# Kernel optimization log

Hardware: AMD Instinct MI355X
Metric: run time of the kernel (lower is better)

## Reference

```python
import jax, jax.numpy as jnp
import numpy as np

E, T, A, H = 64, 128, 32, 4
S, O, QH1, QD, C1 = 256, 128, 128, 64, 128  # state, obs, query hidden, query/key dim, c hidden


def setup_inputs() -> dict:
    key = jax.random.key(0)
    ks = jax.random.split(key, 10)
    w = 0.02
    return {
        "q_values": jax.random.normal(ks[0], (E, T, A), jnp.float32),
        "states": jax.random.normal(ks[1], (E, T, S), jnp.float32),
        "individual_fs": jax.random.normal(ks[2], (E, T, A, O), jnp.float32),
        "Wq1": jax.random.normal(ks[3], (S, QH1), jnp.float32) * w,
        "bq1": jnp.zeros((QH1,), jnp.float32),
        "Wq2": jax.random.normal(ks[4], (QH1, QD), jnp.float32) * w,
        "bq2": jnp.zeros((QD,), jnp.float32),
        "Wk": jax.random.normal(ks[5], (H, O, QD), jnp.float32) * w,
        "bk": jnp.zeros((H, QD), jnp.float32),
        "Wc1": jax.random.normal(ks[6], (S, C1), jnp.float32) * w,
        "bc1": jnp.zeros((C1,), jnp.float32),
        "Wc2": jax.random.normal(ks[7], (C1, 1), jnp.float32) * w,
        "bc2": jnp.zeros((1,), jnp.float32),
    }


def reference(q_values, states, individual_fs, Wq1, bq1, Wq2, bq2, Wk, bk, Wc1, bc1, Wc2, bc2):
    e, t, a = q_values.shape
    s = states.reshape(-1, states.shape[-1])              # (B, S), B = E*T
    f = individual_fs.reshape(e * t, a, -1)               # (B, A, O)
    # query embedding of state: 2-layer MLP with ReLU
    emb_s = jnp.maximum(s @ Wq1 + bq1, 0.0) @ Wq2 + bq2   # (B, QD)
    # all-agents, all-heads key extraction in one batched einsum
    emb_u = jnp.einsum('bao,hok->bahk', f, Wk) + bk       # (B, A, H, QD)
    # query-key dot products per agent/head, then sum over heads
    Lambda_i = jnp.einsum('bk,bahk->bah', emb_s, emb_u).sum(axis=-1)  # (B, A)
    # state-dependent scalar bias
    c_value = jnp.maximum(s @ Wc1 + bc1, 0.0) @ Wc2 + bc2  # (B, 1)
    Q_tot = jnp.sum(Lambda_i * q_values.reshape(-1, a), axis=-1, keepdims=True) + c_value
    return Q_tot.reshape(e, t, 1)
```

## Files before the change

### kernel.cpp

```cpp
#include <hip/hip_runtime.h>


static constexpr int Sd  = 256;
static constexpr int Ad  = 32;
static constexpr int Od  = 128;
static constexpr int QH  = 128;
static constexpr int QDd = 64;
static constexpr int C1d = 128;
static constexpr int NB  = 16;

__global__ void qatten_prep(const float* __restrict__ Wk, const float* __restrict__ bk,
                            float* __restrict__ WkT, float* __restrict__ bkSum)
{
    int idx = blockIdx.x * 256 + threadIdx.x;
    int k = idx >> 7;
    int o = idx & 127;
    float s = 0.f;
#pragma unroll
    for (int h = 0; h < 4; ++h) s += Wk[h * (Od * QDd) + o * QDd + k];
    WkT[k * Od + o] = s;
    if (idx < QDd) {
        float t = 0.f;
#pragma unroll
        for (int h = 0; h < 4; ++h) t += bk[h * QDd + idx];
        bkSum[idx] = t;
    }
}

__global__ __launch_bounds__(256) void qatten_main(
    const float* __restrict__ qv, const float* __restrict__ st, const float* __restrict__ fs,
    const float* __restrict__ Wq1, const float* __restrict__ bq1,
    const float* __restrict__ Wq2, const float* __restrict__ bq2,
    const float* __restrict__ Wc1, const float* __restrict__ bc1,
    const float* __restrict__ Wc2, const float* __restrict__ bc2,
    const float* __restrict__ WkT, const float* __restrict__ bkSum,
    float* __restrict__ out)
{
    __shared__ float s_lds[NB][Sd];
    __shared__ float h1_lds[NB][QH];
    __shared__ float hc_lds[NB][C1d];
    __shared__ float emb_lds[NB][QDd];
    __shared__ float v_lds[NB][Od];
    __shared__ float q_lds[NB][Ad];
    __shared__ float bias_lds[NB];
    __shared__ float part_lds[NB][256];

    const int tid = threadIdx.x;
    const int b0 = blockIdx.x * NB;

    {
        const float4* sp = (const float4*)(st + (size_t)b0 * Sd);
        float4* sl = (float4*)&s_lds[0][0];
#pragma unroll
        for (int i = 0; i < (NB * Sd / 4) / 256; ++i)
            sl[tid + i * 256] = sp[tid + i * 256];
        const float* qp = qv + (size_t)b0 * Ad;
        float* ql = &q_lds[0][0];
#pragma unroll
        for (int i = 0; i < (NB * Ad) / 256; ++i)
            ql[tid + i * 256] = qp[tid + i * 256];
    }
    __syncthreads();

    {
        const int j = tid & 127;
        const bool isC = tid >= 128;
        const float* W  = isC ? Wc1 : Wq1;
        const float* bb = isC ? bc1 : bq1;
        float acc[NB];
#pragma unroll
        for (int b = 0; b < NB; ++b) acc[b] = 0.f;
        for (int i = 0; i < Sd; i += 4) {
            const float w0 = W[(i + 0) * 128 + j];
            const float w1 = W[(i + 1) * 128 + j];
            const float w2 = W[(i + 2) * 128 + j];
            const float w3 = W[(i + 3) * 128 + j];
#pragma unroll
            for (int b = 0; b < NB; ++b) {
                const float4 sv = *(const float4*)&s_lds[b][i];
                float a = acc[b];
                a = fmaf(sv.x, w0, a);
                a = fmaf(sv.y, w1, a);
                a = fmaf(sv.z, w2, a);
                a = fmaf(sv.w, w3, a);
                acc[b] = a;
            }
        }
        const float bias = bb[j];
        float* dst = isC ? &hc_lds[0][0] : &h1_lds[0][0];
#pragma unroll
        for (int b = 0; b < NB; ++b)
            dst[b * 128 + j] = fmaxf(acc[b] + bias, 0.f);
    }
    __syncthreads();

    {
        const int k = tid & 63;
        const int bg = tid >> 6;
        float acc[4] = {0.f, 0.f, 0.f, 0.f};
        for (int j = 0; j < QH; ++j) {
            const float w = Wq2[j * QDd + k];
#pragma unroll
            for (int r = 0; r < 4; ++r)
                acc[r] = fmaf(h1_lds[bg + 4 * r][j], w, acc[r]);
        }
        const float bias = bq2[k];
#pragma unroll
        for (int r = 0; r < 4; ++r)
            emb_lds[bg + 4 * r][k] = acc[r] + bias;
    }
    __syncthreads();

    {
        const int o = tid & 127;
        const int bg = tid >> 7;
        float acc[8] = {0.f,0.f,0.f,0.f,0.f,0.f,0.f,0.f};
        for (int k = 0; k < QDd; ++k) {
            const float w = WkT[k * Od + o];
#pragma unroll
            for (int r = 0; r < 8; ++r)
                acc[r] = fmaf(emb_lds[bg + 2 * r][k], w, acc[r]);
        }
#pragma unroll
        for (int r = 0; r < 8; ++r)
            v_lds[bg + 2 * r][o] = acc[r];
    }
    __syncthreads();

    {
        const int b = tid >> 4;
        const int i = tid & 15;
        float pb = 0.f, pc = 0.f, pq = 0.f;
#pragma unroll
        for (int k = i; k < QDd; k += 16) pb = fmaf(emb_lds[b][k], bkSum[k], pb);
#pragma unroll
        for (int j = i; j < C1d; j += 16) pc = fmaf(hc_lds[b][j], Wc2[j], pc);
        pq = q_lds[b][i] + q_lds[b][i + 16];
#pragma unroll
        for (int d = 8; d >= 1; d >>= 1) {
            pb += __shfl_down(pb, d, 16);
            pc += __shfl_down(pc, d, 16);
            pq += __shfl_down(pq, d, 16);
        }
        if (i == 0) bias_lds[b] = (pc + bc2[0]) + pb * pq;
    }
    __syncthreads();

    {
        const int oq = tid & 31;
        const int ag = tid >> 5;
#pragma unroll 4
        for (int b = 0; b < NB; ++b) {
            const float4* fb = (const float4*)(fs + ((size_t)(b0 + b)) * (Ad * Od));
            const float4 v4 = *(const float4*)&v_lds[b][oq * 4];
            float accb = 0.f;
#pragma unroll
            for (int r = 0; r < 4; ++r) {
                const int a = ag + 8 * r;
                const float4 f4 = fb[a * 32 + oq];
                const float dot = f4.x * v4.x + f4.y * v4.y + f4.z * v4.z + f4.w * v4.w;
                accb = fmaf(q_lds[b][a], dot, accb);
            }
            part_lds[b][tid] = accb;
        }
    }
    __syncthreads();

    {
        const int b = tid >> 4;
        const int i = tid & 15;
        float sum = 0.f;
#pragma unroll
        for (int c = i; c < 256; c += 16) sum += part_lds[b][c];
#pragma unroll
        for (int d = 8; d >= 1; d >>= 1) sum += __shfl_down(sum, d, 16);
        if (i == 0) out[b0 + b] = sum + bias_lds[b];
    }
}

extern "C" void kernel_launch(void* const* d_in, const int* in_sizes, int n_in,
                              void* d_out, int out_size, void* d_ws, size_t ws_size,
                              hipStream_t stream) {
    const float* qv  = (const float*)d_in[0];
    const float* st  = (const float*)d_in[1];
    const float* fs  = (const float*)d_in[2];
    const float* Wq1 = (const float*)d_in[3];
    const float* bq1 = (const float*)d_in[4];
    const float* Wq2 = (const float*)d_in[5];
    const float* bq2 = (const float*)d_in[6];
    const float* Wk  = (const float*)d_in[7];
    const float* bk  = (const float*)d_in[8];
    const float* Wc1 = (const float*)d_in[9];
    const float* bc1 = (const float*)d_in[10];
    const float* Wc2 = (const float*)d_in[11];
    const float* bc2 = (const float*)d_in[12];
    float* out = (float*)d_out;

    float* WkT   = (float*)d_ws;
    float* bkSum = WkT + QDd * Od;

    qatten_prep<<<32, 256, 0, stream>>>(Wk, bk, WkT, bkSum);
    qatten_main<<<512, 256, 0, stream>>>(qv, st, fs, Wq1, bq1, Wq2, bq2,
                                         Wc1, bc1, Wc2, bc2, WkT, bkSum, out);
}
```

Measured before the change: 264.9 us.

## Split fused kernel into MLP kernel and bandwidth-bound feature streaming kernel

The single fused kernel is split into two. The first runs the state MLPs with 32 rows per block and register tiling of two or four columns per thread, then writes the per-row key vectors and scalar bias to workspace. The second streams the large individual_fs tensor with 8 rows per block across 1024 blocks, so more blocks are in flight for the memory-bound part. The cost is an extra launch and a small round trip through global memory for the intermediate vectors.

```diff
diff --git a/kernel.cpp b/kernel.cpp
--- a/kernel.cpp
+++ b/kernel.cpp
@@ -4,10 +4,12 @@
 static constexpr int Sd  = 256;
 static constexpr int Ad  = 32;
 static constexpr int Od  = 128;
-static constexpr int QH  = 128;
 static constexpr int QDd = 64;
-static constexpr int C1d = 128;
-static constexpr int NB  = 16;
+
+static constexpr size_t WS_WKT   = 0;
+static constexpr size_t WS_BKSUM = 8192;
+static constexpr size_t WS_BIAS  = 8256;
+static constexpr size_t WS_V     = 16448;
 
 __global__ void qatten_prep(const float* __restrict__ Wk, const float* __restrict__ bk,
                             float* __restrict__ WkT, float* __restrict__ bkSum)
@@ -27,154 +29,211 @@
     }
 }
 
-__global__ __launch_bounds__(256) void qatten_main(
-    const float* __restrict__ qv, const float* __restrict__ st, const float* __restrict__ fs,
+__global__ __launch_bounds__(256) void qatten_mlp(
+    const float* __restrict__ qv, const float* __restrict__ st,
     const float* __restrict__ Wq1, const float* __restrict__ bq1,
     const float* __restrict__ Wq2, const float* __restrict__ bq2,
     const float* __restrict__ Wc1, const float* __restrict__ bc1,
     const float* __restrict__ Wc2, const float* __restrict__ bc2,
     const float* __restrict__ WkT, const float* __restrict__ bkSum,
+    float* __restrict__ v_ws, float* __restrict__ bias_ws)
+{
+    __shared__ float s_lds[32][Sd];
+    __shared__ float h_lds[32][260];
+    __shared__ float emb_lds[32][QDd];
+
+    const int tid = threadIdx.x;
+    const int b0 = blockIdx.x * 32;
+
+    {
+        const float4* sp = (const float4*)(st + (size_t)b0 * Sd);
+        float4* sl = (float4*)&s_lds[0][0];
+#pragma unroll
+        for (int i = 0; i < 8; ++i) sl[tid + i * 256] = sp[tid + i * 256];
+    }
+    __syncthreads();
+
+    {
+        const int jq = tid & 127;
+        const int rg = tid >> 7;
+        const int c2 = jq * 2;
+        const float* W  = (c2 < 128) ? (Wq1 + c2) : (Wc1 + (c2 - 128));
+        const float* bb = (c2 < 128) ? (bq1 + c2) : (bc1 + (c2 - 128));
+        float acc0[16], acc1[16];
+#pragma unroll
+        for (int r = 0; r < 16; ++r) { acc0[r] = 0.f; acc1[r] = 0.f; }
+        for (int i = 0; i < Sd; i += 4) {
+            const float2 w0 = *(const float2*)(W + (size_t)(i + 0) * 128);
+            const float2 w1 = *(const float2*)(W + (size_t)(i + 1) * 128);
+            const float2 w2 = *(const float2*)(W + (size_t)(i + 2) * 128);
+            const float2 w3 = *(const float2*)(W + (size_t)(i + 3) * 128);
+#pragma unroll
+            for (int r = 0; r < 16; ++r) {
+                const float4 sv = *(const float4*)&s_lds[rg * 16 + r][i];
+                float a0 = acc0[r], a1 = acc1[r];
+                a0 = fmaf(sv.x, w0.x, a0);  a1 = fmaf(sv.x, w0.y, a1);
+                a0 = fmaf(sv.y, w1.x, a0);  a1 = fmaf(sv.y, w1.y, a1);
+                a0 = fmaf(sv.z, w2.x, a0);  a1 = fmaf(sv.z, w2.y, a1);
+                a0 = fmaf(sv.w, w3.x, a0);  a1 = fmaf(sv.w, w3.y, a1);
+                acc0[r] = a0; acc1[r] = a1;
+            }
+        }
+        const float bv0 = bb[0], bv1 = bb[1];
+#pragma unroll
+        for (int r = 0; r < 16; ++r) {
+            float2 hv;
+            hv.x = fmaxf(acc0[r] + bv0, 0.f);
+            hv.y = fmaxf(acc1[r] + bv1, 0.f);
+            *(float2*)&h_lds[rg * 16 + r][c2] = hv;
+        }
+    }
+    __syncthreads();
+
+    {
+        const int jq = tid & 15;
+        const int rg = tid >> 4;
+        const int c4 = jq * 4;
+        float acc[2][4] = {};
+        for (int i = 0; i < 128; i += 4) {
+            const float4 w0 = *(const float4*)(Wq2 + (size_t)(i + 0) * 64 + c4);
+            const float4 w1 = *(const float4*)(Wq2 + (size_t)(i + 1) * 64 + c4);
+            const float4 w2 = *(const float4*)(Wq2 + (size_t)(i + 2) * 64 + c4);
+            const float4 w3 = *(const float4*)(Wq2 + (size_t)(i + 3) * 64 + c4);
+#pragma unroll
+            for (int r = 0; r < 2; ++r) {
+                const float4 hv = *(const float4*)&h_lds[rg * 2 + r][i];
+                acc[r][0] = fmaf(hv.x, w0.x, acc[r][0]);
+                acc[r][1] = fmaf(hv.x, w0.y, acc[r][1]);
+                acc[r][2] = fmaf(hv.x, w0.z, acc[r][2]);
+                acc[r][3] = fmaf(hv.x, w0.w, acc[r][3]);
+                acc[r][0] = fmaf(hv.y, w1.x, acc[r][0]);
+                acc[r][1] = fmaf(hv.y, w1.y, acc[r][1]);
+                acc[r][2] = fmaf(hv.y, w1.z, acc[r][2]);
+                acc[r][3] = fmaf(hv.y, w1.w, acc[r][3]);
+                acc[r][0] = fmaf(hv.z, w2.x, acc[r][0]);
+                acc[r][1] = fmaf(hv.z, w2.y, acc[r][1]);
+                acc[r][2] = fmaf(hv.z, w2.z, acc[r][2]);
+                acc[r][3] = fmaf(hv.z, w2.w, acc[r][3]);
+                acc[r][0] = fmaf(hv.w, w3.x, acc[r][0]);
+                acc[r][1] = fmaf(hv.w, w3.y, acc[r][1]);
+                acc[r][2] = fmaf(hv.w, w3.z, acc[r][2]);
+                acc[r][3] = fmaf(hv.w, w3.w, acc[r][3]);
+            }
+        }
+        const float4 bias = *(const float4*)(bq2 + c4);
+#pragma unroll
+        for (int r = 0; r < 2; ++r) {
+            float4 ev;
+            ev.x = acc[r][0] + bias.x;
+            ev.y = acc[r][1] + bias.y;
+            ev.z = acc[r][2] + bias.z;
+            ev.w = acc[r][3] + bias.w;
+            *(float4*)&emb_lds[rg * 2 + r][c4] = ev;
+        }
+    }
+    __syncthreads();
+
+    {
+        const int jq = tid & 63;
+        const int rg = tid >> 6;
+        const int c2 = jq * 2;
+        float acc0[8], acc1[8];
+#pragma unroll
+        for (int r = 0; r < 8; ++r) { acc0[r] = 0.f; acc1[r] = 0.f; }
+        for (int i = 0; i < QDd; i += 4) {
+            const float2 w0 = *(const float2*)(WkT + (size_t)(i + 0) * 128 + c2);
+            const float2 w1 = *(const float2*)(WkT + (size_t)(i + 1) * 128 + c2);
+            const float2 w2 = *(const float2*)(WkT + (size_t)(i + 2) * 128 + c2);
+            const float2 w3 = *(const float2*)(WkT + (size_t)(i + 3) * 128 + c2);
+#pragma unroll
+            for (int r = 0; r < 8; ++r) {
+                const float4 ev = *(const float4*)&emb_lds[rg * 8 + r][i];
+                float a0 = acc0[r], a1 = acc1[r];
+                a0 = fmaf(ev.x, w0.x, a0);  a1 = fmaf(ev.x, w0.y, a1);
+                a0 = fmaf(ev.y, w1.x, a0);  a1 = fmaf(ev.y, w1.y, a1);
+                a0 = fmaf(ev.z, w2.x, a0);  a1 = fmaf(ev.z, w2.y, a1);
+                a0 = fmaf(ev.w, w3.x, a0);  a1 = fmaf(ev.w, w3.y, a1);
+                acc0[r] = a0; acc1[r] = a1;
+            }
+        }
+#pragma unroll
+        for (int r = 0; r < 8; ++r) {
+            float2 vv; vv.x = acc0[r]; vv.y = acc1[r];
+            *(float2*)(v_ws + (size_t)(b0 + rg * 8 + r) * 128 + c2) = vv;
+        }
+    }
+
+    {
+        const int b = tid >> 3;
+        const int i = tid & 7;
+        float pb = 0.f, pc = 0.f, pq = 0.f;
+#pragma unroll
+        for (int k = i; k < QDd; k += 8)  pb = fmaf(emb_lds[b][k], bkSum[k], pb);
+#pragma unroll
+        for (int j = i; j < 128; j += 8)  pc = fmaf(h_lds[b][128 + j], Wc2[j], pc);
+#pragma unroll
+        for (int a = i; a < Ad; a += 8)   pq += qv[(size_t)(b0 + b) * Ad + a];
+#pragma unroll
+        for (int d = 4; d >= 1; d >>= 1) {
+            pb += __shfl_down(pb, d, 8);
+            pc += __shfl_down(pc, d, 8);
+            pq += __shfl_down(pq, d, 8);
+        }
+        if (i == 0) bias_ws[b0 + b] = (pc + bc2[0]) + pb * pq;
+    }
+}
+
+__global__ __launch_bounds__(256) void qatten_stream(
+    const float* __restrict__ qv, const float* __restrict__ fs,
+    const float* __restrict__ v_ws, const float* __restrict__ bias_ws,
     float* __restrict__ out)
 {
-    __shared__ float s_lds[NB][Sd];
-    __shared__ float h1_lds[NB][QH];
-    __shared__ float hc_lds[NB][C1d];
-    __shared__ float emb_lds[NB][QDd];
-    __shared__ float v_lds[NB][Od];
-    __shared__ float q_lds[NB][Ad];
-    __shared__ float bias_lds[NB];
-    __shared__ float part_lds[NB][256];
+    __shared__ float v_lds[8][Od];
+    __shared__ float q_lds[8][Ad];
+    __shared__ float part_lds[8][256];
 
     const int tid = threadIdx.x;
-    const int b0 = blockIdx.x * NB;
-
-    {
-        const float4* sp = (const float4*)(st + (size_t)b0 * Sd);
-        float4* sl = (float4*)&s_lds[0][0];
-#pragma unroll
-        for (int i = 0; i < (NB * Sd / 4) / 256; ++i)
-            sl[tid + i * 256] = sp[tid + i * 256];
-        const float* qp = qv + (size_t)b0 * Ad;
-        float* ql = &q_lds[0][0];
-#pragma unroll
-        for (int i = 0; i < (NB * Ad) / 256; ++i)
-            ql[tid + i * 256] = qp[tid + i * 256];
-    }
-    __syncthreads();
-
-    {
-        const int j = tid & 127;
-        const bool isC = tid >= 128;
-        const float* W  = isC ? Wc1 : Wq1;
-        const float* bb = isC ? bc1 : bq1;
-        float acc[NB];
-#pragma unroll
-        for (int b = 0; b < NB; ++b) acc[b] = 0.f;
-        for (int i = 0; i < Sd; i += 4) {
-            const float w0 = W[(i + 0) * 128 + j];
-            const float w1 = W[(i + 1) * 128 + j];
-            const float w2 = W[(i + 2) * 128 + j];
-            const float w3 = W[(i + 3) * 128 + j];
-#pragma unroll
-            for (int b = 0; b < NB; ++b) {
-                const float4 sv = *(const float4*)&s_lds[b][i];
-                float a = acc[b];
-                a = fmaf(sv.x, w0, a);
-                a = fmaf(sv.y, w1, a);
-                a = fmaf(sv.z, w2, a);
-                a = fmaf(sv.w, w3, a);
-                acc[b] = a;
-            }
-        }
-        const float bias = bb[j];
-        float* dst = isC ? &hc_lds[0][0] : &h1_lds[0][0];
-#pragma unroll
-        for (int b = 0; b < NB; ++b)
-            dst[b * 128 + j] = fmaxf(acc[b] + bias, 0.f);
-    }
-    __syncthreads();
-
-    {
-        const int k = tid & 63;
-        const int bg = tid >> 6;
-        float acc[4] = {0.f, 0.f, 0.f, 0.f};
-        for (int j = 0; j < QH; ++j) {
-            const float w = Wq2[j * QDd + k];
-#pragma unroll
-            for (int r = 0; r < 4; ++r)
-                acc[r] = fmaf(h1_lds[bg + 4 * r][j], w, acc[r]);
-        }
-        const float bias = bq2[k];
-#pragma unroll
-        for (int r = 0; r < 4; ++r)
-            emb_lds[bg + 4 * r][k] = acc[r] + bias;
-    }
-    __syncthreads();
-
-    {
-        const int o = tid & 127;
-        const int bg = tid >> 7;
-        float acc[8] = {0.f,0.f,0.f,0.f,0.f,0.f,0.f,0.f};
-        for (int k = 0; k < QDd; ++k) {
-            const float w = WkT[k * Od + o];
-#pragma unroll
-            for (int r = 0; r < 8; ++r)
-                acc[r] = fmaf(emb_lds[bg + 2 * r][k], w, acc[r]);
-        }
-#pragma unroll
-        for (int r = 0; r < 8; ++r)
-            v_lds[bg + 2 * r][o] = acc[r];
-    }
-    __syncthreads();
-
-    {
-        const int b = tid >> 4;
-        const int i = tid & 15;
-        float pb = 0.f, pc = 0.f, pq = 0.f;
-#pragma unroll
-        for (int k = i; k < QDd; k += 16) pb = fmaf(emb_lds[b][k], bkSum[k], pb);
-#pragma unroll
-        for (int j = i; j < C1d; j += 16) pc = fmaf(hc_lds[b][j], Wc2[j], pc);
-        pq = q_lds[b][i] + q_lds[b][i + 16];
-#pragma unroll
-        for (int d = 8; d >= 1; d >>= 1) {
-            pb += __shfl_down(pb, d, 16);
-            pc += __shfl_down(pc, d, 16);
-            pq += __shfl_down(pq, d, 16);
-        }
-        if (i == 0) bias_lds[b] = (pc + bc2[0]) + pb * pq;
-    }
+    const int b0 = blockIdx.x * 8;
+
+    ((float4*)&v_lds[0][0])[tid] = ((const float4*)(v_ws + (size_t)b0 * Od))[tid];
+    (&q_lds[0][0])[tid] = qv[(size_t)b0 * Ad + tid];
     __syncthreads();
 
     {
         const int oq = tid & 31;
         const int ag = tid >> 5;
-#pragma unroll 4
-        for (int b = 0; b < NB; ++b) {
-            const float4* fb = (const float4*)(fs + ((size_t)(b0 + b)) * (Ad * Od));
+        float acc[8];
+#pragma unroll
+        for (int b = 0; b < 8; ++b) {
+            const float4* fb = (const float4*)(fs + (size_t)(b0 + b) * (Ad * Od));
             const float4 v4 = *(const float4*)&v_lds[b][oq * 4];
-            float accb = 0.f;
+            float s = 0.f;
 #pragma unroll
             for (int r = 0; r < 4; ++r) {
                 const int a = ag + 8 * r;
                 const float4 f4 = fb[a * 32 + oq];
-                const float dot = f4.x * v4.x + f4.y * v4.y + f4.z * v4.z + f4.w * v4.w;
-                accb = fmaf(q_lds[b][a], dot, accb);
-            }
-            part_lds[b][tid] = accb;
-        }
-    }
-    __syncthreads();
-
-    {
-        const int b = tid >> 4;
-        const int i = tid & 15;
+                float d = f4.x * v4.x;
+                d = fmaf(f4.y, v4.y, d);
+                d = fmaf(f4.z, v4.z, d);
+                d = fmaf(f4.w, v4.w, d);
+                s = fmaf(q_lds[b][a], d, s);
+            }
+            acc[b] = s;
+        }
+#pragma unroll
+        for (int b = 0; b < 8; ++b) part_lds[b][tid] = acc[b];
+    }
+    __syncthreads();
+
+    {
+        const int b = tid >> 5;
+        const int i = tid & 31;
         float sum = 0.f;
 #pragma unroll
-        for (int c = i; c < 256; c += 16) sum += part_lds[b][c];
-#pragma unroll
-        for (int d = 8; d >= 1; d >>= 1) sum += __shfl_down(sum, d, 16);
-        if (i == 0) out[b0 + b] = sum + bias_lds[b];
+        for (int c = i; c < 256; c += 32) sum += part_lds[b][c];
+#pragma unroll
+        for (int d = 16; d >= 1; d >>= 1) sum += __shfl_down(sum, d, 32);
+        if (i == 0) out[b0 + b] = sum + bias_ws[b0 + b];
     }
 }
 
@@ -196,10 +255,15 @@
     const float* bc2 = (const float*)d_in[12];
     float* out = (float*)d_out;
 
-    float* WkT   = (float*)d_ws;
-    float* bkSum = WkT + QDd * Od;
+    float* ws      = (float*)d_ws;
+    float* WkT     = ws + WS_WKT;
+    float* bkSum   = ws + WS_BKSUM;
+    float* bias_ws = ws + WS_BIAS;
+    float* v_ws    = ws + WS_V;
 
     qatten_prep<<<32, 256, 0, stream>>>(Wk, bk, WkT, bkSum);
-    qatten_main<<<512, 256, 0, stream>>>(qv, st, fs, Wq1, bq1, Wq2, bq2,
-                                         Wc1, bc1, Wc2, bc2, WkT, bkSum, out);
-}
+    qatten_mlp<<<256, 256, 0, stream>>>(qv, st, Wq1, bq1, Wq2, bq2,
+                                        Wc1, bc1, Wc2, bc2, WkT, bkSum,
+                                        v_ws, bias_ws);
+    qatten_stream<<<1024, 256, 0, stream>>>(qv, fs, v_ws, bias_ws, out);
+}
```

Result: slower. 275.0 us (+3.8%).

## Halve rows per block, double grid, and replace LDS partial reduction with wave shuffles

Applied to the files above, without the earlier changes.

Cuts rows per block from 16 to 8 and launches 1024 blocks instead of 512, to give the 256 CUs more blocks and hide latency, with launch bounds asking for 4 blocks per CU. The two hidden-layer buffers are merged into one padded LDS array. The final reduction drops the 16x256 partial-sum LDS buffer for wave-level xor shuffles plus a small per-wave LDS table, and one barrier is removed between the key projection and the bias computation. In exchange, each weight matrix is read from global memory by twice as many blocks, and each weight load is reused over fewer rows.

```diff
diff --git a/kernel.cpp b/kernel.cpp
--- a/kernel.cpp
+++ b/kernel.cpp
@@ -4,10 +4,8 @@
 static constexpr int Sd  = 256;
 static constexpr int Ad  = 32;
 static constexpr int Od  = 128;
-static constexpr int QH  = 128;
 static constexpr int QDd = 64;
-static constexpr int C1d = 128;
-static constexpr int NB  = 16;
+static constexpr int NB  = 8;
 
 __global__ void qatten_prep(const float* __restrict__ Wk, const float* __restrict__ bk,
                             float* __restrict__ WkT, float* __restrict__ bkSum)
@@ -27,7 +25,7 @@
     }
 }
 
-__global__ __launch_bounds__(256) void qatten_main(
+__global__ __launch_bounds__(256, 4) void qatten_fused(
     const float* __restrict__ qv, const float* __restrict__ st, const float* __restrict__ fs,
     const float* __restrict__ Wq1, const float* __restrict__ bq1,
     const float* __restrict__ Wq2, const float* __restrict__ bq2,
@@ -37,13 +35,12 @@
     float* __restrict__ out)
 {
     __shared__ float s_lds[NB][Sd];
-    __shared__ float h1_lds[NB][QH];
-    __shared__ float hc_lds[NB][C1d];
+    __shared__ float h_lds[NB][260];
     __shared__ float emb_lds[NB][QDd];
     __shared__ float v_lds[NB][Od];
     __shared__ float q_lds[NB][Ad];
+    __shared__ float red_lds[NB][4];
     __shared__ float bias_lds[NB];
-    __shared__ float part_lds[NB][256];
 
     const int tid = threadIdx.x;
     const int b0 = blockIdx.x * NB;
@@ -51,96 +48,103 @@
     {
         const float4* sp = (const float4*)(st + (size_t)b0 * Sd);
         float4* sl = (float4*)&s_lds[0][0];
-#pragma unroll
-        for (int i = 0; i < (NB * Sd / 4) / 256; ++i)
-            sl[tid + i * 256] = sp[tid + i * 256];
-        const float* qp = qv + (size_t)b0 * Ad;
-        float* ql = &q_lds[0][0];
-#pragma unroll
-        for (int i = 0; i < (NB * Ad) / 256; ++i)
-            ql[tid + i * 256] = qp[tid + i * 256];
-    }
-    __syncthreads();
-
-    {
-        const int j = tid & 127;
-        const bool isC = tid >= 128;
-        const float* W  = isC ? Wc1 : Wq1;
-        const float* bb = isC ? bc1 : bq1;
+        sl[tid] = sp[tid];
+        sl[tid + 256] = sp[tid + 256];
+        (&q_lds[0][0])[tid] = qv[(size_t)b0 * Ad + tid];
+    }
+    __syncthreads();
+
+    {
+        const float* W  = (tid < 128) ? (Wq1 + tid) : (Wc1 + (tid - 128));
+        const float  bb = (tid < 128) ? bq1[tid] : bc1[tid - 128];
         float acc[NB];
 #pragma unroll
-        for (int b = 0; b < NB; ++b) acc[b] = 0.f;
+        for (int r = 0; r < NB; ++r) acc[r] = 0.f;
+#pragma unroll 4
         for (int i = 0; i < Sd; i += 4) {
-            const float w0 = W[(i + 0) * 128 + j];
-            const float w1 = W[(i + 1) * 128 + j];
-            const float w2 = W[(i + 2) * 128 + j];
-            const float w3 = W[(i + 3) * 128 + j];
-#pragma unroll
-            for (int b = 0; b < NB; ++b) {
-                const float4 sv = *(const float4*)&s_lds[b][i];
-                float a = acc[b];
+            const float w0 = W[(size_t)(i + 0) * 128];
+            const float w1 = W[(size_t)(i + 1) * 128];
+            const float w2 = W[(size_t)(i + 2) * 128];
+            const float w3 = W[(size_t)(i + 3) * 128];
+#pragma unroll
+            for (int r = 0; r < NB; ++r) {
+                const float4 sv = *(const float4*)&s_lds[r][i];
+                float a = acc[r];
                 a = fmaf(sv.x, w0, a);
                 a = fmaf(sv.y, w1, a);
                 a = fmaf(sv.z, w2, a);
                 a = fmaf(sv.w, w3, a);
-                acc[b] = a;
+                acc[r] = a;
             }
         }
-        const float bias = bb[j];
-        float* dst = isC ? &hc_lds[0][0] : &h1_lds[0][0];
-#pragma unroll
-        for (int b = 0; b < NB; ++b)
-            dst[b * 128 + j] = fmaxf(acc[b] + bias, 0.f);
+#pragma unroll
+        for (int r = 0; r < NB; ++r)
+            h_lds[r][tid] = fmaxf(acc[r] + bb, 0.f);
     }
     __syncthreads();
 
     {
         const int k = tid & 63;
-        const int bg = tid >> 6;
+        const int rg = tid >> 6;
+        float a0 = 0.f, a1 = 0.f;
+#pragma unroll 4
+        for (int j = 0; j < 128; j += 4) {
+            const float w0 = Wq2[(size_t)(j + 0) * 64 + k];
+            const float w1 = Wq2[(size_t)(j + 1) * 64 + k];
+            const float w2 = Wq2[(size_t)(j + 2) * 64 + k];
+            const float w3 = Wq2[(size_t)(j + 3) * 64 + k];
+            const float4 h0 = *(const float4*)&h_lds[rg][j];
+            const float4 h1 = *(const float4*)&h_lds[rg + 4][j];
+            a0 = fmaf(h0.x, w0, a0);  a1 = fmaf(h1.x, w0, a1);
+            a0 = fmaf(h0.y, w1, a0);  a1 = fmaf(h1.y, w1, a1);
+            a0 = fmaf(h0.z, w2, a0);  a1 = fmaf(h1.z, w2, a1);
+            a0 = fmaf(h0.w, w3, a0);  a1 = fmaf(h1.w, w3, a1);
+        }
+        const float bias = bq2[k];
+        emb_lds[rg][k] = a0 + bias;
+        emb_lds[rg + 4][k] = a1 + bias;
+    }
+    __syncthreads();
+
+    {
+        const int o = tid & 127;
+        const int rg = (tid >> 7) * 4;
         float acc[4] = {0.f, 0.f, 0.f, 0.f};
-        for (int j = 0; j < QH; ++j) {
-            const float w = Wq2[j * QDd + k];
-#pragma unroll
-            for (int r = 0; r < 4; ++r)
-                acc[r] = fmaf(h1_lds[bg + 4 * r][j], w, acc[r]);
-        }
-        const float bias = bq2[k];
-#pragma unroll
-        for (int r = 0; r < 4; ++r)
-            emb_lds[bg + 4 * r][k] = acc[r] + bias;
-    }
-    __syncthreads();
-
-    {
-        const int o = tid & 127;
-        const int bg = tid >> 7;
-        float acc[8] = {0.f,0.f,0.f,0.f,0.f,0.f,0.f,0.f};
-        for (int k = 0; k < QDd; ++k) {
-            const float w = WkT[k * Od + o];
-#pragma unroll
-            for (int r = 0; r < 8; ++r)
-                acc[r] = fmaf(emb_lds[bg + 2 * r][k], w, acc[r]);
-        }
-#pragma unroll
-        for (int r = 0; r < 8; ++r)
-            v_lds[bg + 2 * r][o] = acc[r];
-    }
-    __syncthreads();
-
-    {
-        const int b = tid >> 4;
-        const int i = tid & 15;
-        float pb = 0.f, pc = 0.f, pq = 0.f;
-#pragma unroll
-        for (int k = i; k < QDd; k += 16) pb = fmaf(emb_lds[b][k], bkSum[k], pb);
-#pragma unroll
-        for (int j = i; j < C1d; j += 16) pc = fmaf(hc_lds[b][j], Wc2[j], pc);
-        pq = q_lds[b][i] + q_lds[b][i + 16];
-#pragma unroll
-        for (int d = 8; d >= 1; d >>= 1) {
-            pb += __shfl_down(pb, d, 16);
-            pc += __shfl_down(pc, d, 16);
-            pq += __shfl_down(pq, d, 16);
+#pragma unroll 4
+        for (int k = 0; k < QDd; k += 4) {
+            const float w0 = WkT[(size_t)(k + 0) * 128 + o];
+            const float w1 = WkT[(size_t)(k + 1) * 128 + o];
+            const float w2 = WkT[(size_t)(k + 2) * 128 + o];
+            const float w3 = WkT[(size_t)(k + 3) * 128 + o];
+#pragma unroll
+            for (int r = 0; r < 4; ++r) {
+                const float4 ev = *(const float4*)&emb_lds[rg + r][k];
+                float a = acc[r];
+                a = fmaf(ev.x, w0, a);
+                a = fmaf(ev.y, w1, a);
+                a = fmaf(ev.z, w2, a);
+                a = fmaf(ev.w, w3, a);
+                acc[r] = a;
+            }
+        }
+#pragma unroll
+        for (int r = 0; r < 4; ++r) v_lds[rg + r][o] = acc[r];
+    }
+
+    {
+        const int b = tid >> 5;
+        const int i = tid & 31;
+        float pb = 0.f, pc = 0.f;
+#pragma unroll
+        for (int k = i; k < QDd; k += 32)  pb = fmaf(emb_lds[b][k], bkSum[k], pb);
+#pragma unroll
+        for (int j = i; j < 128; j += 32)  pc = fmaf(h_lds[b][128 + j], Wc2[j], pc);
+        float pq = q_lds[b][i];
+#pragma unroll
+        for (int d = 16; d >= 1; d >>= 1) {
+            pb += __shfl_down(pb, d, 32);
+            pc += __shfl_down(pc, d, 32);
+            pq += __shfl_down(pq, d, 32);
         }
         if (i == 0) bias_lds[b] = (pc + bc2[0]) + pb * pq;
     }
@@ -149,32 +153,43 @@
     {
         const int oq = tid & 31;
         const int ag = tid >> 5;
-#pragma unroll 4
+        float acc[NB];
+#pragma unroll
         for (int b = 0; b < NB; ++b) {
-            const float4* fb = (const float4*)(fs + ((size_t)(b0 + b)) * (Ad * Od));
+            const float4* fb = (const float4*)(fs + (size_t)(b0 + b) * (Ad * Od));
             const float4 v4 = *(const float4*)&v_lds[b][oq * 4];
-            float accb = 0.f;
+            float s = 0.f;
 #pragma unroll
             for (int r = 0; r < 4; ++r) {
                 const int a = ag + 8 * r;
                 const float4 f4 = fb[a * 32 + oq];
-                const float dot = f4.x * v4.x + f4.y * v4.y + f4.z * v4.z + f4.w * v4.w;
-                accb = fmaf(q_lds[b][a], dot, accb);
+                float d = f4.x * v4.x;
+                d = fmaf(f4.y, v4.y, d);
+                d = fmaf(f4.z, v4.z, d);
+                d = fmaf(f4.w, v4.w, d);
+                s = fmaf(q_lds[b][a], d, s);
             }
-            part_lds[b][tid] = accb;
-        }
-    }
-    __syncthreads();
-
-    {
-        const int b = tid >> 4;
-        const int i = tid & 15;
-        float sum = 0.f;
-#pragma unroll
-        for (int c = i; c < 256; c += 16) sum += part_lds[b][c];
-#pragma unroll
-        for (int d = 8; d >= 1; d >>= 1) sum += __shfl_down(sum, d, 16);
-        if (i == 0) out[b0 + b] = sum + bias_lds[b];
+            acc[b] = s;
+        }
+        const int lane = tid & 63;
+        const int wv = tid >> 6;
+#pragma unroll
+        for (int b = 0; b < NB; ++b) {
+            float s = acc[b];
+#pragma unroll
+            for (int d = 32; d >= 1; d >>= 1) s += __shfl_xor(s, d);
+            acc[b] = s;
+        }
+        if (lane == 0) {
+#pragma unroll
+            for (int b = 0; b < NB; ++b) red_lds[b][wv] = acc[b];
+        }
+    }
+    __syncthreads();
+
+    if (tid < NB) {
+        out[b0 + tid] = red_lds[tid][0] + red_lds[tid][1] +
+                        red_lds[tid][2] + red_lds[tid][3] + bias_lds[tid];
     }
 }
 
@@ -200,6 +215,6 @@
     float* bkSum = WkT + QDd * Od;
 
     qatten_prep<<<32, 256, 0, stream>>>(Wk, bk, WkT, bkSum);
-    qatten_main<<<512, 256, 0, stream>>>(qv, st, fs, Wq1, bq1, Wq2, bq2,
-                                         Wc1, bc1, Wc2, bc2, WkT, bkSum, out);
+    qatten_fused<<<1024, 256, 0, stream>>>(qv, st, fs, Wq1, bq1, Wq2, bq2,
+                                           Wc1, bc1, Wc2, bc2, WkT, bkSum, out);
 }
```

Result: faster. 246.6 us (-6.9%).
